# Kernel tuning notes

Hardware: AMD Instinct MI355X
Metric: run time of the kernel (lower is better)

The kernel has to match this reference:

```python
import jax, jax.numpy as jnp
import numpy as np

EMBED_DIM = 1024
NUM_HEADS = 16
HEAD_DIM = EMBED_DIM // NUM_HEADS


def setup_inputs() -> dict:
    key = jax.random.key(0)
    k1, k2, k3, k4, k5 = jax.random.split(key, 5)
    B, N, D = 2, 2048, EMBED_DIM
    s = 1.0 / np.sqrt(D)
    x = jax.random.normal(k1, (B, N, D), dtype=jnp.float32)
    qkv_w = jax.random.uniform(k2, (3 * D, D), minval=-s, maxval=s, dtype=jnp.float32)
    qkv_b = jax.random.uniform(k3, (3 * D,), minval=-s, maxval=s, dtype=jnp.float32)
    proj_w = jax.random.uniform(k4, (D, D), minval=-s, maxval=s, dtype=jnp.float32)
    proj_b = jax.random.uniform(k5, (D,), minval=-s, maxval=s, dtype=jnp.float32)
    return {"x": x, "qkv_w": qkv_w, "qkv_b": qkv_b, "proj_w": proj_w, "proj_b": proj_b}


def reference(x, qkv_w, qkv_b, proj_w, proj_b):
    B, N, D = x.shape
    H, Hd = NUM_HEADS, HEAD_DIM
    scale = Hd ** (-0.5)
    # QKV projection (torch Linear: x @ W.T + b)
    qkv = x @ qkv_w.T + qkv_b                      # [B, N, 3D]
    q, k, v = jnp.split(qkv, 3, axis=-1)
    def split_heads(t):
        return t.reshape(B, N, H, Hd).transpose(0, 2, 1, 3)  # [B, H, N, Hd]
    q, k, v = map(split_heads, (q, k, v))
    attn = jnp.einsum("bhqd,bhkd->bhqk", q, k) * scale       # [B, H, N, N]
    attn = jax.nn.softmax(attn, axis=-1)
    out = jnp.einsum("bhqk,bhkd->bhqd", attn, v)             # [B, H, N, Hd]
    out = out.transpose(0, 2, 1, 3).reshape(B, N, D)
    return out @ proj_w.T + proj_b
```

## Files before the change

kernel.cpp:

```cpp
#include <hip/hip_runtime.h>
#include <hip/hip_bf16.h>


#define DEV __device__ __forceinline__

typedef __attribute__((ext_vector_type(8))) __bf16 bf16x8;
typedef __attribute__((ext_vector_type(4))) float f32x4;

static DEV unsigned short f2bf(float f) {
  unsigned u = __builtin_bit_cast(unsigned, f);
  u += 0x7FFFu + ((u >> 16) & 1u);
  return (unsigned short)(u >> 16);
}

static DEV unsigned pkhalfup(float lo, float hi) {
  unsigned a = __builtin_bit_cast(unsigned, lo) + 0x8000u;
  unsigned b = __builtin_bit_cast(unsigned, hi) + 0x8000u;
  return (a >> 16) | (b & 0xFFFF0000u);
}

static DEV float fexp2(float x) {
#if __has_builtin(__builtin_amdgcn_exp2f)
  return __builtin_amdgcn_exp2f(x);
#else
  return __expf(x * 0.69314718055994531f);
#endif
}

static DEV float max3(float a, float b, float c) {
  return fmaxf(fmaxf(a, b), c);
}

static DEV void gld16(const void* g, void* l) {
  __builtin_amdgcn_global_load_lds(
      (const __attribute__((address_space(1))) unsigned int*)g,
      (__attribute__((address_space(3))) unsigned int*)l, 16, 0, 0);
}

static DEV f32x4 mfma16(bf16x8 a, bf16x8 b, f32x4 c) {
  return __builtin_amdgcn_mfma_f32_16x16x32_bf16(a, b, c, 0, 0, 0);
}

__global__ void k_conv(const float* __restrict__ x, const float* __restrict__ qw,
                       const float* __restrict__ pw, unsigned short* __restrict__ xb,
                       unsigned short* __restrict__ wqb, unsigned short* __restrict__ pwb) {
  int b = blockIdx.x;
  const float* s;
  unsigned short* d;
  int base;
  if (b < 4096)      { s = x;  d = xb;  base = b; }
  else if (b < 7168) { s = qw; d = wqb; base = b - 4096; }
  else               { s = pw; d = pwb; base = b - 7168; }
  int i = (base * 256 + threadIdx.x) * 4;
  float4 v = *reinterpret_cast<const float4*>(s + i);
  union { unsigned short h[4]; uint2 u; } cv;
  cv.h[0] = f2bf(v.x); cv.h[1] = f2bf(v.y); cv.h[2] = f2bf(v.z); cv.h[3] = f2bf(v.w);
  *reinterpret_cast<uint2*>(d + i) = cv.u;
}

static DEV void gemm_tile(const unsigned short* __restrict__ Asb,
                          const unsigned short* __restrict__ Bsb,
                          int wm, int wn, int fr, int fg, f32x4 (&acc)[4][4]) {
  bf16x8 af[4], bw[4];
#pragma unroll
  for (int m = 0; m < 4; ++m)
    af[m] = *reinterpret_cast<const bf16x8*>(Asb + (wm * 64 + m * 16 + fr) * 32 + fg * 8);
#pragma unroll
  for (int n = 0; n < 4; ++n)
    bw[n] = *reinterpret_cast<const bf16x8*>(Bsb + (wn * 64 + n * 16 + fr) * 32 + fg * 8);
#pragma unroll
  for (int m = 0; m < 4; ++m)
#pragma unroll
    for (int n = 0; n < 4; ++n)
      acc[m][n] = mfma16(af[m], bw[n], acc[m][n]);
}

#define QSTAGE(k0)                                                            \
  {                                                                           \
    _Pragma("unroll")                                                         \
    for (int c = 0; c < 2; ++c) {                                             \
      int bi = c * 4096 + wid * 1024 + lane * 16;                             \
      int row = bi >> 6, ce = (bi & 63) >> 1;                                 \
      gld16(gA + (size_t)row * K + (k0) + ce, As + c * 2048 + wid * 512);     \
      gld16(gW + (size_t)row * K + (k0) + ce, Bs + c * 2048 + wid * 512);     \
    }                                                                         \
  }

__global__ __launch_bounds__(256) void k_qkv(
    const unsigned short* __restrict__ A, const unsigned short* __restrict__ W,
    const float* __restrict__ bias, unsigned short* __restrict__ Qb,
    unsigned short* __restrict__ Kb, unsigned short* __restrict__ Vt) {
  const int K = 1024;
  __shared__ __align__(16) unsigned short As[128 * 32], Bs[128 * 32];
  const int tid = threadIdx.x, lane = tid & 63, wid = tid >> 6;
  const int wm = wid >> 1, wn = wid & 1, fr = lane & 15, fg = lane >> 4;
  const size_t bm = blockIdx.x, bn = blockIdx.y;
  const unsigned short* gA = A + bm * 128 * K;
  const unsigned short* gW = W + bn * 128 * K;
  f32x4 acc[4][4] = {};
  for (int k0 = 0; k0 < K; k0 += 32) {
    QSTAGE(k0);
    __syncthreads();
    gemm_tile(As, Bs, wm, wn, fr, fg, acc);
    __syncthreads();
  }
  const float QSCALE = 0.18033688011112043f;
  float bv[4];
#pragma unroll
  for (int n = 0; n < 4; ++n) bv[n] = bias[bn * 128 + wn * 64 + n * 16 + fr];
#pragma unroll
  for (int m = 0; m < 4; ++m)
#pragma unroll
    for (int n = 0; n < 4; ++n) {
      int f = (int)bn * 128 + wn * 64 + n * 16 + fr;
      int t = f >> 10, d = f & 1023, h = d >> 6, hd = d & 63;
      int token0 = (int)bm * 128 + wm * 64 + m * 16 + fg * 4;
      int b_ = token0 >> 11, nn0 = token0 & 2047;
      size_t bh = (size_t)(b_ * 16 + h);
      float v0 = acc[m][n][0] + bv[n], v1 = acc[m][n][1] + bv[n];
      float v2 = acc[m][n][2] + bv[n], v3 = acc[m][n][3] + bv[n];
      if (t == 0) {
        unsigned short* q = Qb + (bh * 2048 + nn0) * 64 + hd;
        q[0] = f2bf(v0 * QSCALE); q[64] = f2bf(v1 * QSCALE);
        q[128] = f2bf(v2 * QSCALE); q[192] = f2bf(v3 * QSCALE);
      } else if (t == 1) {
        unsigned short* k = Kb + (bh * 2048 + nn0) * 64 + hd;
        k[0] = f2bf(v0); k[64] = f2bf(v1); k[128] = f2bf(v2); k[192] = f2bf(v3);
      } else {
        union { unsigned short h[4]; uint2 u; } pk;
        pk.h[0] = f2bf(v0); pk.h[1] = f2bf(v1);
        pk.h[2] = f2bf(v2); pk.h[3] = f2bf(v3);
        *reinterpret_cast<uint2*>(Vt + (bh * 64 + hd) * 2048 + nn0) = pk.u;
      }
    }
}

static DEV void attn_tile(const unsigned short* __restrict__ Ksb,
                          const unsigned short* __restrict__ Vsb,
                          unsigned short* __restrict__ pw,
                          const bf16x8 (&qf)[2][2], int fr, int fg,
                          const int* kcol, const int* pcol,
                          f32x4 (&accO)[2][4], float (&mrow)[2],
                          float (&lpart)[2]) {
  const int prow = fr * 64;
  f32x4 s[2][4] = {};
  __builtin_amdgcn_s_setprio(1);
#pragma unroll
  for (int nf = 0; nf < 4; ++nf)
#pragma unroll
    for (int ks = 0; ks < 2; ++ks) {
      bf16x8 kf = *reinterpret_cast<const bf16x8*>(&Ksb[(nf * 16 + fr) * 64 + kcol[ks]]);
      s[0][nf] = mfma16(kf, qf[0][ks], s[0][nf]);
      s[1][nf] = mfma16(kf, qf[1][ks], s[1][nf]);
    }
  __builtin_amdgcn_s_setprio(0);
  bf16x8 vf[2][4];
#pragma unroll
  for (int ks = 0; ks < 2; ++ks)
#pragma unroll
    for (int df = 0; df < 4; ++df)
      vf[ks][df] = *reinterpret_cast<const bf16x8*>(&Vsb[(df * 16 + fr) * 64 + kcol[ks]]);
#pragma unroll
  for (int m = 0; m < 2; ++m) {
    float m0 = max3(s[m][0][0], s[m][0][1], s[m][0][2]);
    float m1 = max3(s[m][0][3], s[m][1][0], s[m][1][1]);
    float m2 = max3(s[m][1][2], s[m][1][3], s[m][2][0]);
    float m3 = max3(s[m][2][1], s[m][2][2], s[m][2][3]);
    float m4 = max3(s[m][3][0], s[m][3][1], s[m][3][2]);
    float mymax = fmaxf(max3(m0, m1, m2), max3(m3, m4, s[m][3][3]));
    if (!__all(mymax <= mrow[m] + 8.0f)) {
      float pmax = fmaxf(mymax, __shfl_xor(mymax, 16));
      pmax = fmaxf(pmax, __shfl_xor(pmax, 32));
      float mnew = fmaxf(mrow[m], pmax);
      float sc = fexp2(mrow[m] - mnew);
      mrow[m] = mnew;
      lpart[m] *= sc;
      float scq[4];
#pragma unroll
      for (int r = 0; r < 4; ++r) scq[r] = __shfl(sc, fg * 4 + r);
#pragma unroll
      for (int df = 0; df < 4; ++df)
#pragma unroll
        for (int r = 0; r < 4; ++r) accO[m][df][r] *= scq[r];
    }
    float rsn[4];
#pragma unroll
    for (int nf = 0; nf < 4; ++nf) {
      float p0 = fexp2(s[m][nf][0] - mrow[m]), p1 = fexp2(s[m][nf][1] - mrow[m]);
      float p2 = fexp2(s[m][nf][2] - mrow[m]), p3 = fexp2(s[m][nf][3] - mrow[m]);
      uint2 pk;
      pk.x = pkhalfup(p0, p1);
      pk.y = pkhalfup(p2, p3);
      rsn[nf] = (p0 + p1) + (p2 + p3);
      *reinterpret_cast<uint2*>(&pw[prow + pcol[nf]]) = pk;
    }
    lpart[m] += (rsn[0] + rsn[1]) + (rsn[2] + rsn[3]);
    bf16x8 pf[2];
#pragma unroll
    for (int ks = 0; ks < 2; ++ks)
      pf[ks] = *reinterpret_cast<const bf16x8*>(&pw[prow + kcol[ks]]);
    __builtin_amdgcn_s_setprio(1);
#pragma unroll
    for (int df = 0; df < 4; ++df)
#pragma unroll
      for (int ks = 0; ks < 2; ++ks)
        accO[m][df] = mfma16(pf[ks], vf[ks][df], accO[m][df]);
    __builtin_amdgcn_s_setprio(0);
  }
}

__global__ __launch_bounds__(256) void k_attn(
    const unsigned short* __restrict__ Qb, const unsigned short* __restrict__ Kb,
    const unsigned short* __restrict__ Vt, unsigned short* __restrict__ Ob) {
  __shared__ __align__(16) unsigned short Ks0[64 * 64], Ks1[64 * 64];
  __shared__ __align__(16) unsigned short Vs0[64 * 64], Vs1[64 * 64];
  __shared__ __align__(16) unsigned short p_lds[4][16 * 64];
  const int tid = threadIdx.x, lane = tid & 63, w = tid >> 6;
  const int fr = lane & 15, fg = lane >> 4;
  const int bid = (int)(blockIdx.x & 7) * 64 + (int)(blockIdx.x >> 3);
  const int qt = bid & 15, bh = bid >> 4;
  const unsigned short* Qp = Qb + ((size_t)bh * 2048 + qt * 128 + w * 32) * 64;
  const unsigned short* Kp = Kb + (size_t)bh * 2048 * 64;
  const unsigned short* Vp = Vt + (size_t)bh * 64 * 2048;
  unsigned short* pw = &p_lds[w][0];

  int kcol[2], pcol[4];
#pragma unroll
  for (int ks = 0; ks < 2; ++ks) kcol[ks] = ((ks * 4 + fg) ^ (fr & 7)) * 8;
#pragma unroll
  for (int nf = 0; nf < 4; ++nf)
    pcol[nf] = (((2 * nf + (fg >> 1)) ^ (fr & 7)) * 8) + (fg & 1) * 4;

  const int crow0 = w * 16 + (lane >> 3);
  bf16x8 qf[2][2];
#pragma unroll
  for (int m = 0; m < 2; ++m)
#pragma unroll
    for (int ks = 0; ks < 2; ++ks)
      qf[m][ks] = *reinterpret_cast<const bf16x8*>(
          Qp + (m * 16 + fr) * 64 + ks * 32 + fg * 8);

  f32x4 accO[2][4] = {};
  float mrow[2] = {-1e30f, -1e30f}, lpart[2] = {0.f, 0.f};

#define STAGE(KDST, VDST, kti)                                                \
  {                                                                           \
    const unsigned short* Kt_ = Kp + (kti) * 64 * 64;                         \
    _Pragma("unroll")                                                         \
    for (int j = 0; j < 2; ++j) {                                             \
      int cr = crow0 + j * 8;                                                 \
      int cs = (lane & 7) ^ (cr & 7);                                         \
      gld16(Kt_ + cr * 64 + cs * 8, (KDST) + (w * 2 + j) * 512);              \
      gld16(Vp + (size_t)cr * 2048 + (kti) * 64 + cs * 8,                     \
            (VDST) + (w * 2 + j) * 512);                                      \
    }                                                                         \
  }

  STAGE(Ks0, Vs0, 0);
  STAGE(Ks1, Vs1, 1);
  __syncthreads();
  for (int i = 0; i < 16; ++i) {
    attn_tile(Ks0, Vs0, pw, qf, fr, fg, kcol, pcol, accO, mrow, lpart);
    __syncthreads();
    if (i < 15) STAGE(Ks0, Vs0, 2 * i + 2);
    attn_tile(Ks1, Vs1, pw, qf, fr, fg, kcol, pcol, accO, mrow, lpart);
    __syncthreads();
    if (i < 15) STAGE(Ks1, Vs1, 2 * i + 3);
  }
#undef STAGE
  const int b_ = bh >> 4, h = bh & 15;
#pragma unroll
  for (int m = 0; m < 2; ++m) {
    float lrow = lpart[m];
    lrow += __shfl_xor(lrow, 16);
    lrow += __shfl_xor(lrow, 32);
    float linv = 1.f / lrow;
    float lq[4];
#pragma unroll
    for (int r = 0; r < 4; ++r) lq[r] = __shfl(linv, fg * 4 + r);
#pragma unroll
    for (int df = 0; df < 4; ++df)
#pragma unroll
      for (int r = 0; r < 4; ++r) {
        int nn = qt * 128 + w * 32 + m * 16 + fg * 4 + r;
        int d = df * 16 + fr;
        Ob[(size_t)(b_ * 2048 + nn) * 1024 + h * 64 + d] =
            f2bf(accO[m][df][r] * lq[r]);
      }
  }
}

__global__ __launch_bounds__(256) void k_proj(
    const unsigned short* __restrict__ A, const unsigned short* __restrict__ W,
    const float* __restrict__ bias, float* __restrict__ out) {
  const int K = 1024;
  __shared__ __align__(16) unsigned short As[128 * 32], Bs[128 * 32];
  const int tid = threadIdx.x, lane = tid & 63, wid = tid >> 6;
  const int wm = wid >> 1, wn = wid & 1, fr = lane & 15, fg = lane >> 4;
  const size_t bm = blockIdx.x, bn = blockIdx.y;
  const unsigned short* gA = A + bm * 128 * K;
  const unsigned short* gW = W + bn * 128 * K;
  f32x4 acc[4][4] = {};
  for (int k0 = 0; k0 < K; k0 += 32) {
    QSTAGE(k0);
    __syncthreads();
    gemm_tile(As, Bs, wm, wn, fr, fg, acc);
    __syncthreads();
  }
  float bv[4];
#pragma unroll
  for (int n = 0; n < 4; ++n) bv[n] = bias[bn * 128 + wn * 64 + n * 16 + fr];
#pragma unroll
  for (int m = 0; m < 4; ++m)
#pragma unroll
    for (int n = 0; n < 4; ++n)
#pragma unroll
      for (int r = 0; r < 4; ++r) {
        size_t token = bm * 128 + wm * 64 + m * 16 + fg * 4 + r;
        int f = (int)bn * 128 + wn * 64 + n * 16 + fr;
        out[token * 1024 + f] = acc[m][n][r] + bv[n];
      }
}

extern "C" void kernel_launch(void* const* d_in, const int* in_sizes, int n_in,
                              void* d_out, int out_size, void* d_ws, size_t ws_size,
                              hipStream_t stream) {
  const float* x      = (const float*)d_in[0];
  const float* qkv_w  = (const float*)d_in[1];
  const float* qkv_b  = (const float*)d_in[2];
  const float* proj_w = (const float*)d_in[3];
  const float* proj_b = (const float*)d_in[4];
  float* out = (float*)d_out;
  char* ws = (char*)d_ws;
  unsigned short* xb  = (unsigned short*)(ws);
  unsigned short* wqb = (unsigned short*)(ws + (size_t)(8u << 20));
  unsigned short* pwb = (unsigned short*)(ws + (size_t)(14u << 20));
  unsigned short* Qb  = (unsigned short*)(ws + (size_t)(16u << 20));
  unsigned short* Kb  = (unsigned short*)(ws + (size_t)(24u << 20));
  unsigned short* Vt  = (unsigned short*)(ws + (size_t)(32u << 20));
  unsigned short* Ob  = (unsigned short*)(ws + (size_t)(40u << 20));

  k_conv<<<8192, 256, 0, stream>>>(x, qkv_w, proj_w, xb, wqb, pwb);
  k_qkv<<<dim3(32, 24), 256, 0, stream>>>(xb, wqb, qkv_b, Qb, Kb, Vt);
  k_attn<<<512, 256, 0, stream>>>(Qb, Kb, Vt, Ob);
  k_proj<<<dim3(32, 8), 256, 0, stream>>>(Ob, pwb, proj_b, out);
}
```

Before: 194.4 us.

## Stage V transpose through LDS, shrink attention blocks, remap GEMM block order

The QKV GEMM epilogue for V tiles now goes through shared memory as a transpose and writes 16-byte coalesced rows to Vt, where before it scattered 8-byte stores. The attention kernel moves from 4-wave blocks over 128 queries to 2-wave blocks over 64 queries, doubling the grid to 1024 blocks for better occupancy and balance, at the cost of reloading K/V twice as often per query. Both GEMMs switch to a 1D grid with an XCD-aware block remap aimed at L2 locality. V is rounded half-up rather than round-to-nearest-even, and the staging buffer is larger, so shared memory use rises.

```diff
diff --git a/kernel.cpp b/kernel.cpp
--- a/kernel.cpp
+++ b/kernel.cpp
@@ -91,10 +91,13 @@
     const float* __restrict__ bias, unsigned short* __restrict__ Qb,
     unsigned short* __restrict__ Kb, unsigned short* __restrict__ Vt) {
   const int K = 1024;
-  __shared__ __align__(16) unsigned short As[128 * 32], Bs[128 * 32];
+  __shared__ __align__(16) unsigned short smem[8704];
+  unsigned short* As = smem;
+  unsigned short* Bs = smem + 4096;
   const int tid = threadIdx.x, lane = tid & 63, wid = tid >> 6;
   const int wm = wid >> 1, wn = wid & 1, fr = lane & 15, fg = lane >> 4;
-  const size_t bm = blockIdx.x, bn = blockIdx.y;
+  const int vid = (int)(blockIdx.x & 7) * 96 + (int)(blockIdx.x >> 3);
+  const size_t bm = vid / 24, bn = vid % 24;
   const unsigned short* gA = A + bm * 128 * K;
   const unsigned short* gW = W + bn * 128 * K;
   f32x4 acc[4][4] = {};
@@ -108,31 +111,63 @@
   float bv[4];
 #pragma unroll
   for (int n = 0; n < 4; ++n) bv[n] = bias[bn * 128 + wn * 64 + n * 16 + fr];
-#pragma unroll
-  for (int m = 0; m < 4; ++m)
-#pragma unroll
-    for (int n = 0; n < 4; ++n) {
-      int f = (int)bn * 128 + wn * 64 + n * 16 + fr;
-      int t = f >> 10, d = f & 1023, h = d >> 6, hd = d & 63;
-      int token0 = (int)bm * 128 + wm * 64 + m * 16 + fg * 4;
-      int b_ = token0 >> 11, nn0 = token0 & 2047;
-      size_t bh = (size_t)(b_ * 16 + h);
-      float v0 = acc[m][n][0] + bv[n], v1 = acc[m][n][1] + bv[n];
-      float v2 = acc[m][n][2] + bv[n], v3 = acc[m][n][3] + bv[n];
-      if (t == 0) {
-        unsigned short* q = Qb + (bh * 2048 + nn0) * 64 + hd;
-        q[0] = f2bf(v0 * QSCALE); q[64] = f2bf(v1 * QSCALE);
-        q[128] = f2bf(v2 * QSCALE); q[192] = f2bf(v3 * QSCALE);
-      } else if (t == 1) {
-        unsigned short* k = Kb + (bh * 2048 + nn0) * 64 + hd;
-        k[0] = f2bf(v0); k[64] = f2bf(v1); k[128] = f2bf(v2); k[192] = f2bf(v3);
-      } else {
-        union { unsigned short h[4]; uint2 u; } pk;
-        pk.h[0] = f2bf(v0); pk.h[1] = f2bf(v1);
-        pk.h[2] = f2bf(v2); pk.h[3] = f2bf(v3);
-        *reinterpret_cast<uint2*>(Vt + (bh * 64 + hd) * 2048 + nn0) = pk.u;
+  if (bn < 16) {
+#pragma unroll
+    for (int m = 0; m < 4; ++m)
+#pragma unroll
+      for (int n = 0; n < 4; ++n) {
+        int f = (int)bn * 128 + wn * 64 + n * 16 + fr;
+        int t = f >> 10, d = f & 1023, h = d >> 6, hd = d & 63;
+        int token0 = (int)bm * 128 + wm * 64 + m * 16 + fg * 4;
+        int b_ = token0 >> 11, nn0 = token0 & 2047;
+        size_t bh = (size_t)(b_ * 16 + h);
+        float v0 = acc[m][n][0] + bv[n], v1 = acc[m][n][1] + bv[n];
+        float v2 = acc[m][n][2] + bv[n], v3 = acc[m][n][3] + bv[n];
+        if (t == 0) {
+          unsigned short* q = Qb + (bh * 2048 + nn0) * 64 + hd;
+          q[0] = f2bf(v0 * QSCALE); q[64] = f2bf(v1 * QSCALE);
+          q[128] = f2bf(v2 * QSCALE); q[192] = f2bf(v3 * QSCALE);
+        } else {
+          unsigned short* k = Kb + (bh * 2048 + nn0) * 64 + hd;
+          k[0] = f2bf(v0); k[64] = f2bf(v1); k[128] = f2bf(v2); k[192] = f2bf(v3);
+        }
       }
+  } else {
+    unsigned short* vxp = smem;
+    const int d0 = ((int)bn - 16) * 128;
+    const int token0 = (int)bm * 128;
+    const int b_ = token0 >> 11, nnb = token0 & 2047;
+    const int row = tid >> 2, qr = tid & 3;
+#pragma unroll
+    for (int phase = 0; phase < 2; ++phase) {
+      __syncthreads();
+      if (wn == phase) {
+#pragma unroll
+        for (int m = 0; m < 4; ++m)
+#pragma unroll
+          for (int n = 0; n < 4; ++n) {
+            int fl = n * 16 + fr;
+            int tok = wm * 64 + m * 16 + fg * 4;
+            float v0 = acc[m][n][0] + bv[n], v1 = acc[m][n][1] + bv[n];
+            float v2 = acc[m][n][2] + bv[n], v3 = acc[m][n][3] + bv[n];
+            uint2 pk;
+            pk.x = pkhalfup(v0, v1);
+            pk.y = pkhalfup(v2, v3);
+            *reinterpret_cast<uint2*>(&vxp[fl * 136 + tok]) = pk;
+          }
+      }
+      __syncthreads();
+      int d = d0 + phase * 64 + row;
+      int h = d >> 6, hd = d & 63;
+      unsigned short* dst =
+          Vt + ((size_t)(b_ * 16 + h) * 64 + hd) * 2048 + nnb + qr * 32;
+      const unsigned short* src = &vxp[row * 136 + qr * 32];
+#pragma unroll
+      for (int j = 0; j < 4; ++j)
+        *reinterpret_cast<uint4*>(dst + j * 8) =
+            *reinterpret_cast<const uint4*>(src + j * 8);
     }
+  }
 }
 
 static DEV void attn_tile(const unsigned short* __restrict__ Ksb,
@@ -209,17 +244,17 @@
   }
 }
 
-__global__ __launch_bounds__(256) void k_attn(
+__global__ __launch_bounds__(128) void k_attn(
     const unsigned short* __restrict__ Qb, const unsigned short* __restrict__ Kb,
     const unsigned short* __restrict__ Vt, unsigned short* __restrict__ Ob) {
   __shared__ __align__(16) unsigned short Ks0[64 * 64], Ks1[64 * 64];
   __shared__ __align__(16) unsigned short Vs0[64 * 64], Vs1[64 * 64];
-  __shared__ __align__(16) unsigned short p_lds[4][16 * 64];
+  __shared__ __align__(16) unsigned short p_lds[2][16 * 64];
   const int tid = threadIdx.x, lane = tid & 63, w = tid >> 6;
   const int fr = lane & 15, fg = lane >> 4;
-  const int bid = (int)(blockIdx.x & 7) * 64 + (int)(blockIdx.x >> 3);
-  const int qt = bid & 15, bh = bid >> 4;
-  const unsigned short* Qp = Qb + ((size_t)bh * 2048 + qt * 128 + w * 32) * 64;
+  const int bid = (int)(blockIdx.x & 7) * 128 + (int)(blockIdx.x >> 3);
+  const int qt = bid & 31, bh = bid >> 5;
+  const unsigned short* Qp = Qb + ((size_t)bh * 2048 + qt * 64 + w * 32) * 64;
   const unsigned short* Kp = Kb + (size_t)bh * 2048 * 64;
   const unsigned short* Vp = Vt + (size_t)bh * 64 * 2048;
   unsigned short* pw = &p_lds[w][0];
@@ -231,7 +266,7 @@
   for (int nf = 0; nf < 4; ++nf)
     pcol[nf] = (((2 * nf + (fg >> 1)) ^ (fr & 7)) * 8) + (fg & 1) * 4;
 
-  const int crow0 = w * 16 + (lane >> 3);
+  const int crow0 = w * 32 + (lane >> 3);
   bf16x8 qf[2][2];
 #pragma unroll
   for (int m = 0; m < 2; ++m)
@@ -247,12 +282,12 @@
   {                                                                           \
     const unsigned short* Kt_ = Kp + (kti) * 64 * 64;                         \
     _Pragma("unroll")                                                         \
-    for (int j = 0; j < 2; ++j) {                                             \
+    for (int j = 0; j < 4; ++j) {                                             \
       int cr = crow0 + j * 8;                                                 \
       int cs = (lane & 7) ^ (cr & 7);                                         \
-      gld16(Kt_ + cr * 64 + cs * 8, (KDST) + (w * 2 + j) * 512);              \
+      gld16(Kt_ + cr * 64 + cs * 8, (KDST) + (w * 4 + j) * 512);              \
       gld16(Vp + (size_t)cr * 2048 + (kti) * 64 + cs * 8,                     \
-            (VDST) + (w * 2 + j) * 512);                                      \
+            (VDST) + (w * 4 + j) * 512);                                      \
     }                                                                         \
   }
 
@@ -282,7 +317,7 @@
     for (int df = 0; df < 4; ++df)
 #pragma unroll
       for (int r = 0; r < 4; ++r) {
-        int nn = qt * 128 + w * 32 + m * 16 + fg * 4 + r;
+        int nn = qt * 64 + w * 32 + m * 16 + fg * 4 + r;
         int d = df * 16 + fr;
         Ob[(size_t)(b_ * 2048 + nn) * 1024 + h * 64 + d] =
             f2bf(accO[m][df][r] * lq[r]);
@@ -297,7 +332,8 @@
   __shared__ __align__(16) unsigned short As[128 * 32], Bs[128 * 32];
   const int tid = threadIdx.x, lane = tid & 63, wid = tid >> 6;
   const int wm = wid >> 1, wn = wid & 1, fr = lane & 15, fg = lane >> 4;
-  const size_t bm = blockIdx.x, bn = blockIdx.y;
+  const int vid = (int)(blockIdx.x & 7) * 32 + (int)(blockIdx.x >> 3);
+  const size_t bm = vid >> 3, bn = vid & 7;
   const unsigned short* gA = A + bm * 128 * K;
   const unsigned short* gW = W + bn * 128 * K;
   f32x4 acc[4][4] = {};
@@ -341,7 +377,7 @@
   unsigned short* Ob  = (unsigned short*)(ws + (size_t)(40u << 20));
 
   k_conv<<<8192, 256, 0, stream>>>(x, qkv_w, proj_w, xb, wqb, pwb);
-  k_qkv<<<dim3(32, 24), 256, 0, stream>>>(xb, wqb, qkv_b, Qb, Kb, Vt);
-  k_attn<<<512, 256, 0, stream>>>(Qb, Kb, Vt, Ob);
-  k_proj<<<dim3(32, 8), 256, 0, stream>>>(Ob, pwb, proj_b, out);
-}
+  k_qkv<<<768, 256, 0, stream>>>(xb, wqb, qkv_b, Qb, Kb, Vt);
+  k_attn<<<1024, 128, 0, stream>>>(Qb, Kb, Vt, Ob);
+  k_proj<<<256, 256, 0, stream>>>(Ob, pwb, proj_b, out);
+}
```

After: 217.1 us. 1.12x slower.
